# Optimization experiments

Hardware: AMD Instinct MI355X
Metric: run time of the kernel (lower is better)

Reference implementation:

```python
import jax, jax.numpy as jnp
import numpy as np

CDF = 0.9  # sparse_threshold


def setup_inputs() -> dict:
    key = jax.random.key(0)
    ks = jax.random.split(key, 8)
    BS, FPS, PPF, XC, K, YS = 8, 64, 1024, 64, 64, 128
    N = BS * FPS * PPF  # 524288 points
    x = jax.random.normal(ks[0], (N, XC), jnp.float32)
    # locations: cols 0,1 are spatial coords, col 2 is the (sorted) frame id;
    # uniform ragged structure: exactly PPF points per frame.
    frame_id = (jnp.arange(N, dtype=jnp.int32) // PPF)
    loc01 = jax.random.randint(ks[1], (N, 2), 0, 64, dtype=jnp.int32)
    locations = jnp.concatenate([loc01, frame_id[:, None]], axis=1)
    y = jax.random.normal(ks[2], (BS, YS), jnp.float32)
    Wc = jax.random.normal(ks[3], (K, XC), jnp.float32) * 0.05
    bc = jnp.zeros((K,), jnp.float32)
    Wy = jax.random.normal(ks[4], (K, YS), jnp.float32) * 0.05
    Wa = jax.random.normal(ks[5], (1, K), jnp.float32) * 0.05
    ba = jnp.zeros((1,), jnp.float32)
    return {"x": x, "locations": locations, "y": y, "Wc": Wc, "bc": bc,
            "Wy": Wy, "Wa": Wa, "ba": ba,
            "frames_per_sample": FPS, "points_per_frame": PPF}


def reference(x, locations, y, Wc, bc, Wy, Wa, ba, frames_per_sample, points_per_frame):
    N, XC = x.shape
    P = points_per_frame
    T = N // P                       # total frames = sum(x_lens)
    y_k = y @ Wy.T                   # [bs, k]   (y_affine, no bias)
    x_k = x @ Wc.T + bc              # [N, k]    (channel_affine)
    frame_id = locations[:, 2]       # [N]
    batch_id = frame_id // frames_per_sample  # which sample each point belongs to
    # attn_weight_affine(tanh(x_k + y_k[sample]))  -> [N]
    scores = (jnp.tanh(x_k + y_k[batch_id]) @ Wa.T + ba)[:, 0]
    w = jax.nn.softmax(scores.reshape(T, P), axis=-1)  # per-frame softmax
    # top-p (CDF) sparsification per frame: sort desc, cumsum < cdf, keep one more
    order = jnp.argsort(-w, axis=-1)                      # [T, P] desc order
    w_sorted = jnp.take_along_axis(w, order, axis=-1)
    csum = jnp.cumsum(w_sorted, axis=-1)
    keep = jnp.sum(csum < CDF, axis=-1) + 1               # mask[sum(mask)] = True
    rank = jnp.argsort(order, axis=-1)                    # inverse permutation
    mask = (rank < keep[:, None]).reshape(-1)             # [N] bool
    new_x = x[mask, :]
    new_locations = locations[mask, :]
    return new_x, new_locations
```

## Files before the change

kernel.cpp:

```cpp
#include <hip/hip_runtime.h>
#include <math.h>


typedef __attribute__((ext_vector_type(8))) short short8v;
typedef __attribute__((ext_vector_type(4))) float f32x4;

__device__ __forceinline__ unsigned short bf16rne(float f) {
    unsigned u = __builtin_bit_cast(unsigned, f);
    return (unsigned short)((u + 0x7fffu + ((u >> 16) & 1u)) >> 16);
}
__device__ __forceinline__ float bf16f(unsigned short h) {
    unsigned u = ((unsigned)h) << 16;
    return __builtin_bit_cast(float, u);
}

__device__ __forceinline__ float fast_tanh(float z) {
    float az = fabsf(z);
    float e  = __expf(-2.0f * az);
    float r  = (1.0f - e) * __builtin_amdgcn_rcpf(1.0f + e);
    return copysignf(r, z);
}

__global__ __launch_bounds__(512) void prep_kernel(const float* __restrict__ y,
                                                   const float* __restrict__ Wy,
                                                   const float* __restrict__ Wc,
                                                   const float* __restrict__ bc,
                                                   const float* __restrict__ Wa,
                                                   short8v* __restrict__ wfrag,
                                                   float* __restrict__ pre,
                                                   float* __restrict__ waCopy) {
    __shared__ float yks[512];
    const int tid = threadIdx.x;
    {
        const int b = tid >> 6, k = tid & 63;
        const float* yrow = y + b * 128;
        const float* wrow = Wy + k * 128;
        float a0 = 0.f, a1 = 0.f, a2 = 0.f, a3 = 0.f;
#pragma unroll
        for (int j = 0; j < 128; j += 4) {
            a0 += yrow[j + 0] * wrow[j + 0];
            a1 += yrow[j + 1] * wrow[j + 1];
            a2 += yrow[j + 2] * wrow[j + 2];
            a3 += yrow[j + 3] * wrow[j + 3];
        }
        yks[tid] = (a0 + a1) + (a2 + a3);
    }
    __syncthreads();

    for (int f = tid; f < 1536; f += 512) {
        int ln = f & 63, t = f >> 6, kt = t & 3, pc = t >> 2;
        int cs = pc & 1, pr = pc >> 1;
        int k = kt * 16 + (ln & 15), c = cs * 32 + 8 * (ln >> 4);
        const float* wr = Wc + k * 64 + c;
        short8v o;
#pragma unroll
        for (int j = 0; j < 8; ++j) {
            float v = wr[j];
            unsigned short hb = bf16rne(v);
            if (pr == 0) { o[j] = (short)hb; continue; }
            float r1 = v - bf16f(hb);
            unsigned short mb = bf16rne(r1);
            if (pr == 1) { o[j] = (short)mb; continue; }
            float r2 = r1 - bf16f(mb);
            o[j] = (short)bf16rne(r2);
        }
        wfrag[f] = o;
    }
    pre[tid] = bc[tid & 63] + yks[tid];
    if (tid < 64) waCopy[tid] = Wa[tid];
}

__global__ __launch_bounds__(256, 4) void score_kernel(const float* __restrict__ x,
                                                       const short8v* __restrict__ wfrag,
                                                       const float* __restrict__ pre,
                                                       const float* __restrict__ waCopy,
                                                       const float* __restrict__ ba,
                                                       float* __restrict__ scores) {
    __shared__ short8v sWf[1536];
    __shared__ float sPre[64];
    __shared__ float sWaS[64];
    const int tid  = threadIdx.x;
    const int lane = tid & 63;
    const int wv   = tid >> 6;
    const int b    = blockIdx.x >> 9;
    const int pbase = blockIdx.x * 128 + wv * 32;

    const int prow0 = pbase + (lane & 15);
    const int cg = 8 * (lane >> 4);
    float4 u[2][2][2];
#pragma unroll
    for (int pt = 0; pt < 2; ++pt) {
        const float* xr = x + (long long)(prow0 + pt * 16) * 64;
#pragma unroll
        for (int cs = 0; cs < 2; ++cs) {
            const float4* xp4 = (const float4*)(xr + cs * 32 + cg);
            u[pt][cs][0] = xp4[0];
            u[pt][cs][1] = xp4[1];
        }
    }

    for (int f = tid; f < 1536; f += 256) sWf[f] = wfrag[f];
    if (tid < 64) { sPre[tid] = pre[b * 64 + tid]; sWaS[tid] = waCopy[tid]; }
    __syncthreads();

    short8v A[2][3][2];
#pragma unroll
    for (int pt = 0; pt < 2; ++pt) {
#pragma unroll
        for (int cs = 0; cs < 2; ++cs) {
            float4 u0 = u[pt][cs][0], u1 = u[pt][cs][1];
            float v[8] = {u0.x, u0.y, u0.z, u0.w, u1.x, u1.y, u1.z, u1.w};
            short8v h, m, l;
#pragma unroll
            for (int j = 0; j < 8; ++j) {
                float vv = v[j];
                unsigned short hb = (unsigned short)(__builtin_bit_cast(unsigned, vv) >> 16);
                float r1 = vv - bf16f(hb);
                unsigned short mb = (unsigned short)(__builtin_bit_cast(unsigned, r1) >> 16);
                float r2 = r1 - bf16f(mb);
                unsigned short lb = (unsigned short)(__builtin_bit_cast(unsigned, r2) >> 16);
                h[j] = (short)hb; m[j] = (short)mb; l[j] = (short)lb;
            }
            A[pt][0][cs] = h; A[pt][1][cs] = m; A[pt][2][cs] = l;
        }
    }

    f32x4 sacc[2] = {{0.f, 0.f, 0.f, 0.f}, {0.f, 0.f, 0.f, 0.f}};
    const float ba0 = ba[0];
    const int kcol = lane & 15;
#pragma unroll
    for (int kt = 0; kt < 4; ++kt) {
        short8v B[3][2];
#pragma unroll
        for (int pr = 0; pr < 3; ++pr)
#pragma unroll
            for (int cs = 0; cs < 2; ++cs)
                B[pr][cs] = sWf[((pr * 2 + cs) * 4 + kt) * 64 + lane];
        const float prek = sPre[kt * 16 + kcol];
        const float wak = sWaS[kt * 16 + kcol];
#pragma unroll
        for (int pt = 0; pt < 2; ++pt) {
            f32x4 acc = {0.f, 0.f, 0.f, 0.f};
#pragma unroll
            for (int cs = 0; cs < 2; ++cs) {
                acc = __builtin_amdgcn_mfma_f32_16x16x32_bf16(A[pt][2][cs], B[0][cs], acc, 0, 0, 0);
                acc = __builtin_amdgcn_mfma_f32_16x16x32_bf16(A[pt][0][cs], B[2][cs], acc, 0, 0, 0);
                acc = __builtin_amdgcn_mfma_f32_16x16x32_bf16(A[pt][1][cs], B[1][cs], acc, 0, 0, 0);
                acc = __builtin_amdgcn_mfma_f32_16x16x32_bf16(A[pt][1][cs], B[0][cs], acc, 0, 0, 0);
                acc = __builtin_amdgcn_mfma_f32_16x16x32_bf16(A[pt][0][cs], B[1][cs], acc, 0, 0, 0);
                acc = __builtin_amdgcn_mfma_f32_16x16x32_bf16(A[pt][0][cs], B[0][cs], acc, 0, 0, 0);
            }
#pragma unroll
            for (int r = 0; r < 4; ++r) {
                float z = acc[r] + prek;
                sacc[pt][r] += wak * fast_tanh(z);
            }
        }
    }

#pragma unroll
    for (int pt = 0; pt < 2; ++pt)
#pragma unroll
        for (int r = 0; r < 4; ++r) {
            float v = sacc[pt][r];
            v += __shfl_xor(v, 1);
            v += __shfl_xor(v, 2);
            v += __shfl_xor(v, 4);
            v += __shfl_xor(v, 8);
            if (kcol == 0)
                scores[pbase + pt * 16 + (lane >> 4) * 4 + r] = v + ba0;
        }
}

__global__ __launch_bounds__(1024) void tile_kernel(const float* __restrict__ scores,
                                                    int* __restrict__ flags,
                                                    int* __restrict__ keepcnt) {
    const int t = blockIdx.x, tid = threadIdx.x;
    __shared__ float sw[1024];
    __shared__ int   si[1024];
    __shared__ float red[16];
    __shared__ int   keep_s;

    const int lane = tid & 63, wid = tid >> 6;
    float s = scores[t * 1024 + tid];

    float m = s;
#pragma unroll
    for (int o = 32; o; o >>= 1) m = fmaxf(m, __shfl_xor(m, o));
    if (lane == 0) red[wid] = m;
    __syncthreads();
    float mb = red[0];
#pragma unroll
    for (int q = 1; q < 16; ++q) mb = fmaxf(mb, red[q]);
    __syncthreads();

    float e = expf(s - mb);
    float su = e;
#pragma unroll
    for (int o = 32; o; o >>= 1) su += __shfl_xor(su, o);
    if (lane == 0) red[wid] = su;
    __syncthreads();
    float tot = 0.f;
#pragma unroll
    for (int q = 0; q < 16; ++q) tot += red[q];

    float w  = e / tot;
    int   idx = tid;

    for (int kk = 2; kk <= 1024; kk <<= 1) {
        for (int j = kk >> 1; j > 0; j >>= 1) {
            bool lower = (tid & j) == 0;
            bool desc2 = (tid & kk) == 0;
            float wp; int ip;
            if (j >= 64) {
                sw[tid] = w; si[tid] = idx;
                __syncthreads();
                wp = sw[tid ^ j]; ip = si[tid ^ j];
                bool before = (w > wp) || (w == wp && idx < ip);
                bool keep = desc2 ? (before == lower) : (before != lower);
                if (!keep) { w = wp; idx = ip; }
                __syncthreads();
            } else {
                wp = __shfl_xor(w, j);
                ip = __shfl_xor(idx, j);
                bool before = (w > wp) || (w == wp && idx < ip);
                bool keep = desc2 ? (before == lower) : (before != lower);
                if (!keep) { w = wp; idx = ip; }
            }
        }
    }

    sw[tid] = w;
    __syncthreads();

    if (tid == 0) {
        float c = 0.f; int kp = 0;
#pragma unroll 8
        for (int q = 0; q < 1024; ++q) { c += sw[q]; if (c < 0.9f) ++kp; }
        keep_s = kp + 1;
        keepcnt[t] = kp + 1;
    }
    __syncthreads();

    flags[t * 1024 + idx] = (tid < keep_s) ? 1 : 0;
}

__global__ __launch_bounds__(64) void offsets_kernel(const int* __restrict__ keepcnt,
                                                     int* __restrict__ toffs, int T) {
    const int lane = threadIdx.x;
    const int base = lane * 8;
    int v[8]; int s = 0;
#pragma unroll
    for (int j = 0; j < 8; ++j) { v[j] = keepcnt[base + j]; s += v[j]; }
    int inc = s;
#pragma unroll
    for (int o = 1; o < 64; o <<= 1) {
        int tmp = __shfl_up(inc, o);
        if (lane >= o) inc += tmp;
    }
    int r = inc - s;
#pragma unroll
    for (int j = 0; j < 8; ++j) { toffs[base + j] = r; r += v[j]; }
}

__global__ __launch_bounds__(1024) void compact_kernel(const float* __restrict__ x,
                                                       const int* __restrict__ locs,
                                                       const int* __restrict__ flags,
                                                       const int* __restrict__ toffs,
                                                       float* __restrict__ out,
                                                       int M) {
    const int t = blockIdx.x, tid = threadIdx.x;
    const long long gi = (long long)t * 1024 + tid;
    const int f = flags[gi];
    const int lane = tid & 63, wid = tid >> 6;

    unsigned long long ball = __ballot(f != 0);
    int wpre = __popcll(ball & (((unsigned long long)1 << lane) - 1ULL));

    __shared__ int wtot[16];
    __shared__ int woff[16];
    __shared__ int rowsrc[1024];
    __shared__ int nk_s;
    if (lane == 63) wtot[wid] = wpre + f;
    __syncthreads();
    if (tid == 0) {
        int r = 0;
#pragma unroll
        for (int q = 0; q < 16; ++q) { woff[q] = r; r += wtot[q]; }
        nk_s = r;
    }
    __syncthreads();

    const int base = toffs[t];
    if (f) {
        const int local = woff[wid] + wpre;
        rowsrc[local] = tid;
        const long long pos = (long long)base + local;
        float* lout = out + (long long)M * 64 + pos * 3;
        lout[0] = (float)locs[gi * 3 + 0];
        lout[1] = (float)locs[gi * 3 + 1];
        lout[2] = (float)locs[gi * 3 + 2];
    }
    __syncthreads();

    const int nk = nk_s;
    const int rsub = tid >> 4;
    const int col  = tid & 15;
    for (int r0 = 0; r0 < nk; r0 += 64) {
        const int rr = r0 + rsub;
        if (rr < nk) {
            const int srow = rowsrc[rr];
            const float4* src = (const float4*)(x + ((long long)t * 1024 + srow) * 64);
            float4* dst = (float4*)(out + (long long)(base + rr) * 64);
            dst[col] = src[col];
        }
    }
}

extern "C" void kernel_launch(void* const* d_in, const int* in_sizes, int n_in,
                              void* d_out, int out_size, void* d_ws, size_t ws_size,
                              hipStream_t stream) {
    const float* x    = (const float*)d_in[0];
    const int*   locs = (const int*)d_in[1];
    const float* y    = (const float*)d_in[2];
    const float* Wc   = (const float*)d_in[3];
    const float* bc   = (const float*)d_in[4];
    const float* Wy   = (const float*)d_in[5];
    const float* Wa   = (const float*)d_in[6];
    const float* ba   = (const float*)d_in[7];

    const int N = in_sizes[0] / 64;
    const int T = N / 1024;
    const int M = out_size / 67;

    float* ws      = (float*)d_ws;
    float* scores  = ws + 512;
    int*   flags   = (int*)(ws + 512 + N);
    int*   keepcnt = flags + N;
    int*   toffs   = keepcnt + T;
    short8v* wfrag = (short8v*)(ws + 512 + 2 * N + 2 * T);
    float* pre     = ws + 512 + 2 * N + 2 * T + 6144;
    float* waCopy  = pre + 512;

    prep_kernel<<<1, 512, 0, stream>>>(y, Wy, Wc, bc, Wa, wfrag, pre, waCopy);
    score_kernel<<<N / 128, 256, 0, stream>>>(x, wfrag, pre, waCopy, ba, scores);
    tile_kernel<<<T, 1024, 0, stream>>>(scores, flags, keepcnt);
    offsets_kernel<<<1, 64, 0, stream>>>(keepcnt, toffs, T);
    compact_kernel<<<T, 1024, 0, stream>>>(x, locs, flags, toffs, (float*)d_out, M);
}
```

Baseline: 134.2 us.

## Fuse score computation into per-frame tile kernel, keep scores in shared memory

Merges the MFMA-based score kernel into the per-frame softmax/sort kernel. Each 1024-thread block now computes its frame's 1024 scores into shared memory and sorts them directly, which removes the global scores round trip and one kernel launch. The trade-off is 512 blocks of 1024 threads instead of 4096 blocks of 256 threads, so occupancy drops and the x loads can no longer overlap with another kernel's sort phase. Each wave also processes two 32-point slabs in sequence.

Result: slower. 292.0 us (+117.5%).

```diff
diff --git a/kernel.cpp b/kernel.cpp
--- a/kernel.cpp
+++ b/kernel.cpp
@@ -70,124 +70,127 @@
     if (tid < 64) waCopy[tid] = Wa[tid];
 }
 
-__global__ __launch_bounds__(256, 4) void score_kernel(const float* __restrict__ x,
-                                                       const short8v* __restrict__ wfrag,
-                                                       const float* __restrict__ pre,
-                                                       const float* __restrict__ waCopy,
-                                                       const float* __restrict__ ba,
-                                                       float* __restrict__ scores) {
+__global__ __launch_bounds__(1024) void score_tile_kernel(const float* __restrict__ x,
+                                                          const short8v* __restrict__ wfrag,
+                                                          const float* __restrict__ pre,
+                                                          const float* __restrict__ waCopy,
+                                                          const float* __restrict__ ba,
+                                                          int* __restrict__ flags,
+                                                          int* __restrict__ keepcnt) {
     __shared__ short8v sWf[1536];
     __shared__ float sPre[64];
     __shared__ float sWaS[64];
-    const int tid  = threadIdx.x;
-    const int lane = tid & 63;
-    const int wv   = tid >> 6;
-    const int b    = blockIdx.x >> 9;
-    const int pbase = blockIdx.x * 128 + wv * 32;
-
-    const int prow0 = pbase + (lane & 15);
-    const int cg = 8 * (lane >> 4);
-    float4 u[2][2][2];
-#pragma unroll
-    for (int pt = 0; pt < 2; ++pt) {
-        const float* xr = x + (long long)(prow0 + pt * 16) * 64;
-#pragma unroll
-        for (int cs = 0; cs < 2; ++cs) {
-            const float4* xp4 = (const float4*)(xr + cs * 32 + cg);
-            u[pt][cs][0] = xp4[0];
-            u[pt][cs][1] = xp4[1];
-        }
-    }
-
-    for (int f = tid; f < 1536; f += 256) sWf[f] = wfrag[f];
-    if (tid < 64) { sPre[tid] = pre[b * 64 + tid]; sWaS[tid] = waCopy[tid]; }
-    __syncthreads();
-
-    short8v A[2][3][2];
-#pragma unroll
-    for (int pt = 0; pt < 2; ++pt) {
-#pragma unroll
-        for (int cs = 0; cs < 2; ++cs) {
-            float4 u0 = u[pt][cs][0], u1 = u[pt][cs][1];
-            float v[8] = {u0.x, u0.y, u0.z, u0.w, u1.x, u1.y, u1.z, u1.w};
-            short8v h, m, l;
-#pragma unroll
-            for (int j = 0; j < 8; ++j) {
-                float vv = v[j];
-                unsigned short hb = (unsigned short)(__builtin_bit_cast(unsigned, vv) >> 16);
-                float r1 = vv - bf16f(hb);
-                unsigned short mb = (unsigned short)(__builtin_bit_cast(unsigned, r1) >> 16);
-                float r2 = r1 - bf16f(mb);
-                unsigned short lb = (unsigned short)(__builtin_bit_cast(unsigned, r2) >> 16);
-                h[j] = (short)hb; m[j] = (short)mb; l[j] = (short)lb;
-            }
-            A[pt][0][cs] = h; A[pt][1][cs] = m; A[pt][2][cs] = l;
-        }
-    }
-
-    f32x4 sacc[2] = {{0.f, 0.f, 0.f, 0.f}, {0.f, 0.f, 0.f, 0.f}};
-    const float ba0 = ba[0];
-    const int kcol = lane & 15;
-#pragma unroll
-    for (int kt = 0; kt < 4; ++kt) {
-        short8v B[3][2];
-#pragma unroll
-        for (int pr = 0; pr < 3; ++pr)
-#pragma unroll
-            for (int cs = 0; cs < 2; ++cs)
-                B[pr][cs] = sWf[((pr * 2 + cs) * 4 + kt) * 64 + lane];
-        const float prek = sPre[kt * 16 + kcol];
-        const float wak = sWaS[kt * 16 + kcol];
-#pragma unroll
-        for (int pt = 0; pt < 2; ++pt) {
-            f32x4 acc = {0.f, 0.f, 0.f, 0.f};
-#pragma unroll
-            for (int cs = 0; cs < 2; ++cs) {
-                acc = __builtin_amdgcn_mfma_f32_16x16x32_bf16(A[pt][2][cs], B[0][cs], acc, 0, 0, 0);
-                acc = __builtin_amdgcn_mfma_f32_16x16x32_bf16(A[pt][0][cs], B[2][cs], acc, 0, 0, 0);
-                acc = __builtin_amdgcn_mfma_f32_16x16x32_bf16(A[pt][1][cs], B[1][cs], acc, 0, 0, 0);
-                acc = __builtin_amdgcn_mfma_f32_16x16x32_bf16(A[pt][1][cs], B[0][cs], acc, 0, 0, 0);
-                acc = __builtin_amdgcn_mfma_f32_16x16x32_bf16(A[pt][0][cs], B[1][cs], acc, 0, 0, 0);
-                acc = __builtin_amdgcn_mfma_f32_16x16x32_bf16(A[pt][0][cs], B[0][cs], acc, 0, 0, 0);
-            }
-#pragma unroll
-            for (int r = 0; r < 4; ++r) {
-                float z = acc[r] + prek;
-                sacc[pt][r] += wak * fast_tanh(z);
-            }
-        }
-    }
-
-#pragma unroll
-    for (int pt = 0; pt < 2; ++pt)
-#pragma unroll
-        for (int r = 0; r < 4; ++r) {
-            float v = sacc[pt][r];
-            v += __shfl_xor(v, 1);
-            v += __shfl_xor(v, 2);
-            v += __shfl_xor(v, 4);
-            v += __shfl_xor(v, 8);
-            if (kcol == 0)
-                scores[pbase + pt * 16 + (lane >> 4) * 4 + r] = v + ba0;
-        }
-}
-
-__global__ __launch_bounds__(1024) void tile_kernel(const float* __restrict__ scores,
-                                                    int* __restrict__ flags,
-                                                    int* __restrict__ keepcnt) {
-    const int t = blockIdx.x, tid = threadIdx.x;
+    __shared__ float sscore[1024];
     __shared__ float sw[1024];
     __shared__ int   si[1024];
     __shared__ float red[16];
     __shared__ int   keep_s;
 
-    const int lane = tid & 63, wid = tid >> 6;
-    float s = scores[t * 1024 + tid];
+    const int tid  = threadIdx.x;
+    const int lane = tid & 63;
+    const int wv   = tid >> 6;
+    const int t    = blockIdx.x;
+    const int b    = t >> 6;
+
+    for (int f = tid; f < 1536; f += 1024) sWf[f] = wfrag[f];
+    if (tid < 64) { sPre[tid] = pre[b * 64 + tid]; sWaS[tid] = waCopy[tid]; }
+    __syncthreads();
+
+    const float ba0 = ba[0];
+    const int kcol = lane & 15;
+
+    for (int ps = 0; ps < 2; ++ps) {
+        const int pl = wv * 64 + ps * 32;
+        const long long pbase = (long long)t * 1024 + pl;
+
+        const long long prow0 = pbase + (lane & 15);
+        const int cg = 8 * (lane >> 4);
+        float4 u[2][2][2];
+#pragma unroll
+        for (int pt = 0; pt < 2; ++pt) {
+            const float* xr = x + (prow0 + pt * 16) * 64;
+#pragma unroll
+            for (int cs = 0; cs < 2; ++cs) {
+                const float4* xp4 = (const float4*)(xr + cs * 32 + cg);
+                u[pt][cs][0] = xp4[0];
+                u[pt][cs][1] = xp4[1];
+            }
+        }
+
+        short8v A[2][3][2];
+#pragma unroll
+        for (int pt = 0; pt < 2; ++pt) {
+#pragma unroll
+            for (int cs = 0; cs < 2; ++cs) {
+                float4 u0 = u[pt][cs][0], u1 = u[pt][cs][1];
+                float v[8] = {u0.x, u0.y, u0.z, u0.w, u1.x, u1.y, u1.z, u1.w};
+                short8v h, m, l;
+#pragma unroll
+                for (int j = 0; j < 8; ++j) {
+                    float vv = v[j];
+                    unsigned short hb = (unsigned short)(__builtin_bit_cast(unsigned, vv) >> 16);
+                    float r1 = vv - bf16f(hb);
+                    unsigned short mb = (unsigned short)(__builtin_bit_cast(unsigned, r1) >> 16);
+                    float r2 = r1 - bf16f(mb);
+                    unsigned short lb = (unsigned short)(__builtin_bit_cast(unsigned, r2) >> 16);
+                    h[j] = (short)hb; m[j] = (short)mb; l[j] = (short)lb;
+                }
+                A[pt][0][cs] = h; A[pt][1][cs] = m; A[pt][2][cs] = l;
+            }
+        }
+
+        f32x4 sacc[2] = {{0.f, 0.f, 0.f, 0.f}, {0.f, 0.f, 0.f, 0.f}};
+#pragma unroll
+        for (int kt = 0; kt < 4; ++kt) {
+            short8v B[3][2];
+#pragma unroll
+            for (int pr = 0; pr < 3; ++pr)
+#pragma unroll
+                for (int cs = 0; cs < 2; ++cs)
+                    B[pr][cs] = sWf[((pr * 2 + cs) * 4 + kt) * 64 + lane];
+            const float prek = sPre[kt * 16 + kcol];
+            const float wak = sWaS[kt * 16 + kcol];
+#pragma unroll
+            for (int pt = 0; pt < 2; ++pt) {
+                f32x4 acc = {0.f, 0.f, 0.f, 0.f};
+#pragma unroll
+                for (int cs = 0; cs < 2; ++cs) {
+                    acc = __builtin_amdgcn_mfma_f32_16x16x32_bf16(A[pt][2][cs], B[0][cs], acc, 0, 0, 0);
+                    acc = __builtin_amdgcn_mfma_f32_16x16x32_bf16(A[pt][0][cs], B[2][cs], acc, 0, 0, 0);
+                    acc = __builtin_amdgcn_mfma_f32_16x16x32_bf16(A[pt][1][cs], B[1][cs], acc, 0, 0, 0);
+                    acc = __builtin_amdgcn_mfma_f32_16x16x32_bf16(A[pt][1][cs], B[0][cs], acc, 0, 0, 0);
+                    acc = __builtin_amdgcn_mfma_f32_16x16x32_bf16(A[pt][0][cs], B[1][cs], acc, 0, 0, 0);
+                    acc = __builtin_amdgcn_mfma_f32_16x16x32_bf16(A[pt][0][cs], B[0][cs], acc, 0, 0, 0);
+                }
+#pragma unroll
+                for (int r = 0; r < 4; ++r) {
+                    float z = acc[r] + prek;
+                    sacc[pt][r] += wak * fast_tanh(z);
+                }
+            }
+        }
+
+#pragma unroll
+        for (int pt = 0; pt < 2; ++pt)
+#pragma unroll
+            for (int r = 0; r < 4; ++r) {
+                float v = sacc[pt][r];
+                v += __shfl_xor(v, 1);
+                v += __shfl_xor(v, 2);
+                v += __shfl_xor(v, 4);
+                v += __shfl_xor(v, 8);
+                if (kcol == 0)
+                    sscore[pl + pt * 16 + (lane >> 4) * 4 + r] = v + ba0;
+            }
+    }
+    __syncthreads();
+
+    float s = sscore[tid];
 
     float m = s;
 #pragma unroll
     for (int o = 32; o; o >>= 1) m = fmaxf(m, __shfl_xor(m, o));
-    if (lane == 0) red[wid] = m;
+    if (lane == 0) red[wv] = m;
     __syncthreads();
     float mb = red[0];
 #pragma unroll
@@ -198,7 +201,7 @@
     float su = e;
 #pragma unroll
     for (int o = 32; o; o >>= 1) su += __shfl_xor(su, o);
-    if (lane == 0) red[wid] = su;
+    if (lane == 0) red[wv] = su;
     __syncthreads();
     float tot = 0.f;
 #pragma unroll
@@ -334,7 +337,6 @@
     const int M = out_size / 67;
 
     float* ws      = (float*)d_ws;
-    float* scores  = ws + 512;
     int*   flags   = (int*)(ws + 512 + N);
     int*   keepcnt = flags + N;
     int*   toffs   = keepcnt + T;
@@ -343,8 +345,7 @@
     float* waCopy  = pre + 512;
 
     prep_kernel<<<1, 512, 0, stream>>>(y, Wy, Wc, bc, Wa, wfrag, pre, waCopy);
-    score_kernel<<<N / 128, 256, 0, stream>>>(x, wfrag, pre, waCopy, ba, scores);
-    tile_kernel<<<T, 1024, 0, stream>>>(scores, flags, keepcnt);
+    score_tile_kernel<<<T, 1024, 0, stream>>>(x, wfrag, pre, waCopy, ba, flags, keepcnt);
     offsets_kernel<<<1, 64, 0, stream>>>(keepcnt, toffs, T);
     compact_kernel<<<T, 1024, 0, stream>>>(x, locs, flags, toffs, (float*)d_out, M);
 }
```
